# Kernel tuning notes

Measured on AMD Instinct MI355X. Metric: run time of the kernel, lower is better.

## Reference

```python
import jax, jax.numpy as jnp
import numpy as np

L = 4          # num_layers
H = 128        # hidden_channels
F = 128        # num_filters
G = 25         # num_gaussians
N = 10000      # nodes
E = 320000     # radius-graph edges
EH = 40000     # hull edges
NG = 64        # graphs in batch
CUTOFF = 5.0
PI = float(np.pi)
LOG2 = float(np.log(2.0))


def ssp(x):  # ShiftedSoftplus
    return jax.nn.softplus(x) - LOG2


def setup_inputs() -> dict:
    key = jax.random.key(0)
    ks = iter(jax.random.split(key, 64))
    w = lambda shape: jax.random.normal(next(ks), shape, jnp.float32) * 0.05
    inp = {
        'z': jax.random.randint(next(ks), (N,), 0, 100),
        'edge_index': jax.random.randint(next(ks), (2, E), 0, N),
        'edge_index_hull': jax.random.randint(next(ks), (2, EH), 0, N),
        'batch': jnp.sort(jax.random.randint(next(ks), (N,), 0, NG)),
        'dist': jax.random.uniform(next(ks), (E,), jnp.float32) * CUTOFF,
        'fea_hull': jax.random.normal(next(ks), (EH, 7), jnp.float32),
        'emb_table': w((100, H)),
        'lin_w': w((L, F, H)),
        'mlp_w1': w((L, F, G)), 'mlp_b1': jnp.zeros((L, F), jnp.float32),
        'mlp_w2': w((L, F, F)), 'mlp_b2': jnp.zeros((L, F), jnp.float32),
        'linh_w': w((L, F, H)),
        'mlph_w1': w((L, F, 7)), 'mlph_b1': jnp.zeros((L, F), jnp.float32),
        'mlph_w2': w((L, F, F)), 'mlph_b2': jnp.zeros((L, F), jnp.float32),
        'v1_w': w((L, H, F)), 'v1_b': jnp.zeros((L, H), jnp.float32),
        'v2_w': w((L, 64, H)), 'v2_b': jnp.zeros((L, 64), jnp.float32),
        'vh1_w': w((L, H, F)), 'vh1_b': jnp.zeros((L, H), jnp.float32),
        'vh2_w': w((L, 64, H)), 'vh2_b': jnp.zeros((L, 64), jnp.float32),
        'cat_w': w((L, H, 128)), 'cat_b': jnp.zeros((L, H), jnp.float32),
        'u1_w': w((64, H)), 'u1_b': jnp.zeros((64,), jnp.float32),
        'u2_w': w((1, 64)), 'u2_b': jnp.zeros((1,), jnp.float32),
    }
    return inp


def reference(z, edge_index, edge_index_hull, batch, dist, fea_hull, emb_table,
              lin_w, mlp_w1, mlp_b1, mlp_w2, mlp_b2,
              linh_w, mlph_w1, mlph_b1, mlph_w2, mlph_b2,
              v1_w, v1_b, v2_w, v2_b, vh1_w, vh1_b, vh2_w, vh2_b,
              cat_w, cat_b, u1_w, u1_b, u2_w, u2_b):
    n = z.shape[0]
    # Gaussian distance embedding: emb(0, cutoff, G)
    offset = jnp.linspace(0.0, CUTOFF, G)
    coeff = -0.5 / (offset[1] - offset[0]) ** 2
    dist_emb = jnp.exp(coeff * (dist[:, None] - offset[None, :]) ** 2)  # [E,G]
    C = 0.5 * (jnp.cos(dist * PI / CUTOFF) + 1.0)                       # [E]
    j, i = edge_index[0], edge_index[1]
    jh, ih = edge_index_hull[0], edge_index_hull[1]
    v = emb_table[z]                                                    # [N,H]
    for l in range(L):
        # update_e
        W = (ssp(dist_emb @ mlp_w1[l].T + mlp_b1[l]) @ mlp_w2[l].T + mlp_b2[l]) * C[:, None]
        e = (v @ lin_w[l].T)[j] * W                                     # [E,F]
        Wh = ssp(fea_hull @ mlph_w1[l].T + mlph_b1[l]) @ mlph_w2[l].T + mlph_b2[l]
        eh = (v @ linh_w[l].T)[jh] * Wh                                 # [EH,F]
        # update_v
        out = jax.ops.segment_sum(e, i, num_segments=n)
        out = ssp(out @ v1_w[l].T + v1_b[l]) @ v2_w[l].T + v2_b[l]      # [N,64]
        outh = jax.ops.segment_sum(eh, ih, num_segments=n)
        outh = ssp(outh @ vh1_w[l].T + vh1_b[l]) @ vh2_w[l].T + vh2_b[l]
        v = v + ssp(jnp.concatenate([out, outh], axis=1) @ cat_w[l].T + cat_b[l])
    # update_u
    u = ssp(v @ u1_w.T + u1_b) @ u2_w.T + u2_b                          # [N,1]
    return jax.ops.segment_sum(u, batch, num_segments=NG)               # [NG,1]
```

## Files before the change

kernel.cpp:

```cpp
#include <hip/hip_runtime.h>
#include <hip/hip_bf16.h>

typedef __hip_bfloat16 bf16;
typedef unsigned short ushort;
typedef __attribute__((ext_vector_type(8))) short short8;
typedef __attribute__((ext_vector_type(4))) float f32x4;

__device__ __forceinline__ float dssp(float x){
  return fmaxf(x, 0.f) + __logf(1.f + __expf(-fabsf(x))) - 0.693147180559945f;
}
__device__ __forceinline__ int clampi(int x, int lo, int hi){ return x<lo?lo:(x>hi?hi:x); }
__device__ __forceinline__ ushort f2b(float f){
  unsigned x = __float_as_uint(f);
  return (ushort)((x + 0x7fffu + ((x>>16)&1u)) >> 16);
}
__device__ __forceinline__ float b2f16(ushort u){ return __uint_as_float(((unsigned)u)<<16); }

constexpr int TBL_K    = 4096;
constexpr int TBL_ROWS = TBL_K + 1;
constexpr int TBL_TILES = (TBL_ROWS + 31) / 32;

__global__ void detect_mode(const unsigned* __restrict__ raw, int* flag){
  __shared__ int c;
  int t = threadIdx.x;
  if (t==0) c = 0;
  __syncthreads();
  unsigned u  = raw[t];
  unsigned lo = u & 0xFFFFu;
  int e = (int)((lo >> 7) & 0xFF);
  int ok = (lo==0u) || (e >= 0x70 && e <= 0x8F);
  atomicAdd(&c, ok);
  __syncthreads();
  if (t==0) *flag = (c >= 160) ? 1 : 0;
}

struct Seg { const void* src; float* dst; int n; };
struct SegTable { Seg s[27]; int count; long total; };

__global__ void convert_all(SegTable tbl, const int* __restrict__ flag){
  int mode = *flag;
  long tid    = (long)blockIdx.x*blockDim.x + threadIdx.x;
  long stride = (long)gridDim.x*blockDim.x;
  for (long i=tid; i<tbl.total; i+=stride){
    long off = i; int k = 0;
    while (k < tbl.count-1 && off >= tbl.s[k].n){ off -= tbl.s[k].n; k++; }
    float f;
    if (mode) f = __bfloat162float(((const bf16*)tbl.s[k].src)[off]);
    else      f = ((const float*)tbl.s[k].src)[off];
    tbl.s[k].dst[off] = (f==f) ? f : 0.f;
  }
}

struct WSeg { const float* src; ushort* dst; int n; };
struct WTable { WSeg s[9]; int count; int total; };

__global__ void convert_wb(WTable wt){
  int tid = blockIdx.x*blockDim.x + threadIdx.x;
  if (tid >= wt.total) return;
  int off = tid, k = 0;
  while (k < wt.count-1 && off >= wt.s[k].n){ off -= wt.s[k].n; k++; }
  wt.s[k].dst[off] = f2b(wt.s[k].src[off]);
}

__global__ void init_all(int* cnt_r, int* cnt_h, float* uacc,
                         int2* spk_r, int2* spk_h, int N, int E, int EH){
  int t = blockIdx.x*blockDim.x + threadIdx.x;
  if (t < N){ cnt_r[t]=0; cnt_h[t]=0; }
  if (t < 64) uacc[t]=0.f;
  if (t < E)  spk_r[t]=make_int2(0,0);
  if (t < EH) spk_h[t]=make_int2(0,0);
}

__global__ void count_edges(const int* __restrict__ ei, const int* __restrict__ eih,
                            int E, int EH, int N, int* cnt_r, int* cnt_h){
  int t = blockIdx.x*blockDim.x + threadIdx.x;
  if (t < E)  atomicAdd(&cnt_r[clampi(ei[E + t], 0, N-1)], 1);
  if (t < EH) atomicAdd(&cnt_h[clampi(eih[EH + t], 0, N-1)], 1);
}

__global__ __launch_bounds__(256) void scan_pair(const int* cnt_r, int* off_r, int* cur_r,
                                                 const int* cnt_h, int* off_h, int* cur_h, int N){
  __shared__ int s[256];
  int t = threadIdx.x;
  int CH = (N + 255) / 256;
  for (int which=0; which<2; which++){
    const int* cnt = which? cnt_h : cnt_r;
    int* off = which? off_h : off_r;
    int* cur = which? cur_h : cur_r;
    int base = t*CH;
    int sum = 0;
    for (int q=0;q<CH;q++){ int idx=base+q; sum += (idx<N)? cnt[idx] : 0; }
    __syncthreads();
    s[t]=sum; __syncthreads();
    for (int ofs=1; ofs<256; ofs<<=1){
      int v = s[t]; int vp = (t>=ofs)? s[t-ofs] : 0;
      __syncthreads(); s[t]=v+vp; __syncthreads();
    }
    int run = (t>0)? s[t-1] : 0;
    for (int q=0;q<CH;q++){
      int idx=base+q;
      if (idx<N){ off[idx]=run; cur[idx]=run; run += cnt[idx]; }
    }
    if (t==255) off[N] = s[255];
  }
}

__global__ void scatter_edges(const int* __restrict__ ei, const float* __restrict__ distc,
                              const int* __restrict__ eih, int E, int EH, int N,
                              int* cur_r, int* cur_h, int2* spk_r, int2* spk_h){
  int t = blockIdx.x*blockDim.x + threadIdx.x;
  if (t < E){
    int i = clampi(ei[E+t], 0, N-1);
    int p = clampi(atomicAdd(&cur_r[i], 1), 0, E-1);
    float x = fminf(fmaxf(distc[t]*(4096.0f/5.0f), 0.f), 4095.999f);
    int i0 = (int)x; if (i0 > TBL_K-1) i0 = TBL_K-1;
    unsigned fr16 = (unsigned)((x - (float)i0)*65536.0f); if (fr16 > 65535u) fr16 = 65535u;
    spk_r[p] = make_int2(clampi(ei[t],0,N-1), (int)(((unsigned)i0<<16)|fr16));
  }
  if (t < EH){
    int ih = clampi(eih[EH+t], 0, N-1);
    int p = clampi(atomicAdd(&cur_h[ih], 1), 0, EH-1);
    spk_h[p] = make_int2(clampi(eih[t],0,N-1), t);
  }
}

__global__ __launch_bounds__(256) void build_wtab(const float* __restrict__ mlp_w1,
    const float* __restrict__ mlp_b1, const float* __restrict__ mlp_w2,
    const float* __restrict__ mlp_b2, ushort* __restrict__ Wtab){
  int l    = blockIdx.x / TBL_TILES;
  int tile = blockIdx.x % TBL_TILES;
  int row0 = tile * 32;
  const float* w1 = mlp_w1 + l*128*25;
  const float* b1 = mlp_b1 + l*128;
  const float* w2 = mlp_w2 + l*128*128;
  const float* b2 = mlp_b2 + l*128;
  __shared__ float Gs[32][26];
  __shared__ float Ts[32][129];
  __shared__ float Ws[32][129];
  int t = threadIdx.x;
  for (int idx=t; idx<32*25; idx+=256){
    int r = idx/25, k = idx%25;
    float d = (row0+r) * (5.0f/4096.0f);
    float x = d - (float)k*(5.0f/24.0f);
    Gs[r][k] = __expf(-11.52f*x*x);
  }
  __syncthreads();
  int rg = t&7, cg = t>>3;
  #pragma unroll
  for (int ri=0;ri<4;ri++){
    int r = rg*4+ri;
    #pragma unroll
    for (int ci=0;ci<4;ci++){
      int c = cg*4+ci;
      float s = b1[c];
      for (int k=0;k<25;k++) s += Gs[r][k]*w1[c*25+k];
      Ts[r][c] = dssp(s);
    }
  }
  float acc[4][4] = {};
  for (int k0=0;k0<128;k0+=32){
    __syncthreads();
    for (int idx=t; idx<1024; idx+=256){
      int c=idx>>3, kk4=(idx&7)*4;
      float4 f = *(const float4*)(w2+(size_t)c*128+k0+kk4);
      Ws[kk4][c]=f.x; Ws[kk4+1][c]=f.y; Ws[kk4+2][c]=f.z; Ws[kk4+3][c]=f.w;
    }
    __syncthreads();
    for (int kk=0;kk<32;kk++){
      float xv[4];
      #pragma unroll
      for (int ri=0;ri<4;ri++) xv[ri]=Ts[rg*4+ri][k0+kk];
      #pragma unroll
      for (int ci=0;ci<4;ci++){
        float wv = Ws[kk][cg*4+ci];
        #pragma unroll
        for (int ri=0;ri<4;ri++) acc[ri][ci] += xv[ri]*wv;
      }
    }
  }
  #pragma unroll
  for (int ri=0;ri<4;ri++){
    int r = row0 + rg*4 + ri;
    if (r >= TBL_ROWS) continue;
    float d  = r * (5.0f/4096.0f);
    float Cf = 0.5f*(cosf(d*(3.14159265358979f/5.0f))+1.0f);
    #pragma unroll
    for (int ci=0;ci<4;ci++){
      int c = cg*4+ci;
      Wtab[((size_t)l*TBL_ROWS + r)*128 + c] = f2b((acc[ri][ci] + b2[c]) * Cf);
    }
  }
}

__global__ void pack_wtab(const ushort* __restrict__ Wtab, unsigned* __restrict__ Wpk){
  long t = (long)blockIdx.x*blockDim.x + threadIdx.x;
  const long TOT = 4L*TBL_K*128;
  if (t < TOT){
    int l = (int)(t / ((long)TBL_K*128));
    long rem = t % ((long)TBL_K*128);
    int r = (int)(rem >> 7), f = (int)(rem & 127);
    const ushort* base = Wtab + (size_t)l*TBL_ROWS*128;
    Wpk[t] = (((unsigned)base[(size_t)(r+1)*128+f])<<16) | (unsigned)base[(size_t)r*128+f];
  }
}

__device__ __forceinline__ short8 afragb(const ushort (*Xb)[136], int lane, int k0){
  int m=lane&15, q=(lane>>4)&3;
  return *(const short8*)(&Xb[m][k0+q*8]);
}
__device__ __forceinline__ short8 bfrag(const ushort* __restrict__ W, int cbase, int lane, int k0){
  int n=lane&15, q=(lane>>4)&3;
  return *(const short8*)(W + (size_t)(cbase+n)*128 + k0 + q*8);
}
template<int NT>
__device__ __forceinline__ void mgemm(const ushort (*Xb)[136],
    const ushort* __restrict__ W, int t, f32x4 d[NT]){
  int lane=t&63, w=t>>6;
  #pragma unroll
  for (int ct=0;ct<NT;ct++) d[ct]=(f32x4){0.f,0.f,0.f,0.f};
  #pragma unroll
  for (int kc=0;kc<4;kc++){
    short8 a = afragb(Xb, lane, kc*32);
    #pragma unroll
    for (int ct=0;ct<NT;ct++){
      short8 b = bfrag(W, w*(NT*16)+ct*16, lane, kc*32);
      d[ct] = __builtin_amdgcn_mfma_f32_16x16x32_bf16(a, b, d[ct], 0, 0, 0);
    }
  }
}
template<int NT>
__device__ __forceinline__ void d2tile(ushort (*Y)[136], const f32x4 d[NT], int t,
    int colofs, const float* __restrict__ bias, int do_ssp){
  int lane=t&63, w=t>>6, q=(lane>>4)&3, n=lane&15;
  #pragma unroll
  for (int ct=0;ct<NT;ct++){
    int c = w*(NT*16)+ct*16+n;
    float bv = bias? bias[c] : 0.f;
    #pragma unroll
    for (int i=0;i<4;i++){
      float y = d[ct][i] + bv;
      if (do_ssp) y = dssp(y);
      Y[q*4+i][colofs+c] = f2b(y);
    }
  }
}
template<int NT>
__device__ __forceinline__ void d2os(float (*Os)[132], const f32x4 d[NT], int t,
    const float* __restrict__ bias, int do_ssp){
  int lane=t&63, w=t>>6, q=(lane>>4)&3, n=lane&15;
  #pragma unroll
  for (int ct=0;ct<NT;ct++){
    int c = w*(NT*16)+ct*16+n;
    float bv = bias? bias[c] : 0.f;
    #pragma unroll
    for (int i=0;i<4;i++){
      float y = d[ct][i] + bv;
      if (do_ssp) y = dssp(y);
      Os[q*4+i][c] = y;
    }
  }
}
__device__ __forceinline__ void d2glob(ushort* __restrict__ out, const f32x4 d[2],
    int t, int row0, int N){
  int lane=t&63, w=t>>6, q=(lane>>4)&3, n=lane&15;
  #pragma unroll
  for (int ct=0;ct<2;ct++){
    int c = w*32+ct*16+n;
    #pragma unroll
    for (int i=0;i<4;i++){
      int gr = row0 + q*4 + i;
      if (gr<N) out[(size_t)gr*128 + c] = f2b(d[ct][i]);
    }
  }
}

__global__ __launch_bounds__(256) void f_first(const int* __restrict__ z,
    const float* __restrict__ emb, float* __restrict__ v,
    const ushort* __restrict__ linA, const ushort* __restrict__ linB,
    ushort* __restrict__ vlin, ushort* __restrict__ vlinh, int N){
  __shared__ ushort Xb[16][136];
  int t=threadIdx.x; int row0=blockIdx.x*16;
  f32x4 d[2];
  for (int idx=t; idx<512; idx+=256){
    int r=idx>>5, k4=(idx&31)*4; int gr=row0+r;
    int zz=(gr<N)? clampi(z[gr],0,99):0;
    float4 f = *(const float4*)(emb + (size_t)zz*128 + k4);
    unsigned r0 = (unsigned)f2b(f.x) | ((unsigned)f2b(f.y)<<16);
    unsigned r1 = (unsigned)f2b(f.z) | ((unsigned)f2b(f.w)<<16);
    *(uint2*)&Xb[r][k4] = make_uint2(r0,r1);
    if (gr<N) *(float4*)(v + (size_t)gr*128 + k4) = f;
  }
  __syncthreads();
  mgemm<2>(Xb, linA, t, d);
  d2glob(vlin, d, t, row0, N);
  mgemm<2>(Xb, linB, t, d);
  d2glob(vlinh, d, t, row0, N);
}

__global__ __launch_bounds__(256) void f_mid(
    const float* __restrict__ accR, const float* __restrict__ accH,
    float* __restrict__ v,
    const ushort* __restrict__ v1w, const float* __restrict__ v1b,
    const ushort* __restrict__ v2w, const float* __restrict__ v2b,
    const ushort* __restrict__ vh1w, const float* __restrict__ vh1b,
    const ushort* __restrict__ vh2w, const float* __restrict__ vh2b,
    const ushort* __restrict__ cw, const float* __restrict__ cb,
    const ushort* __restrict__ linA, const ushort* __restrict__ linB,
    ushort* __restrict__ vlin, ushort* __restrict__ vlinh, int N){
  __shared__ ushort Xb[16][136];
  __shared__ ushort Xb2[16][136];
  __shared__ ushort Xb3[16][136];
  __shared__ float  Os[16][132];
  int t=threadIdx.x; int row0=blockIdx.x*16;
  f32x4 d[2]; f32x4 d1[1];

  for (int path=0; path<2; path++){
    const float* X = path? accH : accR;
    __syncthreads();
    for (int idx=t; idx<512; idx+=256){
      int r=idx>>5, k4=(idx&31)*4; int gr=row0+r;
      float4 f=(gr<N)? *(const float4*)(X+(size_t)gr*128+k4):make_float4(0,0,0,0);
      unsigned r0 = (unsigned)f2b(f.x) | ((unsigned)f2b(f.y)<<16);
      unsigned r1 = (unsigned)f2b(f.z) | ((unsigned)f2b(f.w)<<16);
      *(uint2*)&Xb[r][k4] = make_uint2(r0,r1);
    }
    __syncthreads();
    mgemm<2>(Xb, path?vh1w:v1w, t, d);
    d2tile<2>(Xb2, d, t, 0, path?vh1b:v1b, 1);
    __syncthreads();
    mgemm<1>(Xb2, path?vh2w:v2w, t, d1);
    d2tile<1>(Xb3, d1, t, path*64, path?vh2b:v2b, 0);
  }
  __syncthreads();
  mgemm<2>(Xb3, cw, t, d);
  d2os<2>(Os, d, t, cb, 1);
  __syncthreads();
  for (int idx=t; idx<512; idx+=256){
    int r=idx>>5, k4=(idx&31)*4; int gr=row0+r;
    float4 f=(gr<N)? *(const float4*)(v+(size_t)gr*128+k4):make_float4(0,0,0,0);
    f.x+=Os[r][k4]; f.y+=Os[r][k4+1]; f.z+=Os[r][k4+2]; f.w+=Os[r][k4+3];
    if (gr<N) *(float4*)(v+(size_t)gr*128+k4)=f;
    unsigned r0 = (unsigned)f2b(f.x) | ((unsigned)f2b(f.y)<<16);
    unsigned r1 = (unsigned)f2b(f.z) | ((unsigned)f2b(f.w)<<16);
    *(uint2*)&Xb[r][k4] = make_uint2(r0,r1);
  }
  __syncthreads();
  mgemm<2>(Xb, linA, t, d);
  d2glob(vlin, d, t, row0, N);
  mgemm<2>(Xb, linB, t, d);
  d2glob(vlinh, d, t, row0, N);
}

__global__ __launch_bounds__(256) void f_last(
    const float* __restrict__ accR, const float* __restrict__ accH,
    const float* __restrict__ v,
    const ushort* __restrict__ v1w, const float* __restrict__ v1b,
    const ushort* __restrict__ v2w, const float* __restrict__ v2b,
    const ushort* __restrict__ vh1w, const float* __restrict__ vh1b,
    const ushort* __restrict__ vh2w, const float* __restrict__ vh2b,
    const ushort* __restrict__ cw, const float* __restrict__ cb,
    const ushort* __restrict__ u1w, const float* __restrict__ u1b,
    const float* __restrict__ u2w, const float* __restrict__ u2b,
    const int* __restrict__ batch, float* __restrict__ uacc, int N){
  __shared__ ushort Xb[16][136];
  __shared__ ushort Xb2[16][136];
  __shared__ ushort Xb3[16][136];
  __shared__ float  Os[16][132];
  __shared__ float ss[16];
  __shared__ int   bb[16];
  int t=threadIdx.x; int row0=blockIdx.x*16;
  f32x4 d[2]; f32x4 d1[1];

  for (int path=0; path<2; path++){
    const float* X = path? accH : accR;
    __syncthreads();
    for (int idx=t; idx<512; idx+=256){
      int r=idx>>5, k4=(idx&31)*4; int gr=row0+r;
      float4 f=(gr<N)? *(const float4*)(X+(size_t)gr*128+k4):make_float4(0,0,0,0);
      unsigned r0 = (unsigned)f2b(f.x) | ((unsigned)f2b(f.y)<<16);
      unsigned r1 = (unsigned)f2b(f.z) | ((unsigned)f2b(f.w)<<16);
      *(uint2*)&Xb[r][k4] = make_uint2(r0,r1);
    }
    __syncthreads();
    mgemm<2>(Xb, path?vh1w:v1w, t, d);
    d2tile<2>(Xb2, d, t, 0, path?vh1b:v1b, 1);
    __syncthreads();
    mgemm<1>(Xb2, path?vh2w:v2w, t, d1);
    d2tile<1>(Xb3, d1, t, path*64, path?vh2b:v2b, 0);
  }
  __syncthreads();
  mgemm<2>(Xb3, cw, t, d);
  d2os<2>(Os, d, t, cb, 1);
  __syncthreads();
  for (int idx=t; idx<512; idx+=256){
    int r=idx>>5, k4=(idx&31)*4; int gr=row0+r;
    float4 f=(gr<N)? *(const float4*)(v+(size_t)gr*128+k4):make_float4(0,0,0,0);
    f.x+=Os[r][k4]; f.y+=Os[r][k4+1]; f.z+=Os[r][k4+2]; f.w+=Os[r][k4+3];
    unsigned r0 = (unsigned)f2b(f.x) | ((unsigned)f2b(f.y)<<16);
    unsigned r1 = (unsigned)f2b(f.z) | ((unsigned)f2b(f.w)<<16);
    *(uint2*)&Xb[r][k4] = make_uint2(r0,r1);
  }
  __syncthreads();
  mgemm<1>(Xb, u1w, t, d1);
  d2os<1>(Os, d1, t, u1b, 1);
  __syncthreads();
  if (t<16){
    int gr=row0+t;
    float s=0.f; int bt=-1;
    if (gr<N){
      s = u2b[0];
      for (int c=0;c<64;c++) s += Os[t][c]*u2w[c];
      bt = clampi(batch[gr],0,63);
    }
    ss[t]=s; bb[t]=bt;
  }
  __syncthreads();
  if (t==0){
    float run=0.f; int cur=-1;
    for (int q=0;q<16;q++){
      int bq=bb[q];
      if (bq<0) continue;
      if (bq!=cur){ if (cur>=0) atomicAdd(&uacc[cur],run); cur=bq; run=0.f; }
      run += ss[q];
    }
    if (cur>=0) atomicAdd(&uacc[cur],run);
  }
}

__global__ __launch_bounds__(256) void hull_all(const int2* __restrict__ spk_h,
    const float* __restrict__ fea,
    const float* __restrict__ mlph_w1, const float* __restrict__ mlph_b1,
    const ushort* __restrict__ mlph_w2b, const float* __restrict__ mlph_b2,
    ushort* __restrict__ WhT_base, size_t lstride, int EHpad,
    int EH, int tilesPerLayer, int l0){
  int l    = l0 + blockIdx.x / tilesPerLayer;
  int tile = blockIdx.x % tilesPerLayer;
  int row0 = tile*64;
  const float* w1 = mlph_w1 + l*128*7;
  const float* b1 = mlph_b1 + l*128;
  const ushort* w2 = mlph_w2b + (size_t)l*16384;
  const float* b2 = mlph_b2 + l*128;
  ushort* WhT = WhT_base + (size_t)(l-l0)*lstride;
  __shared__ float Fs[64][8];
  __shared__ ushort Xb[64][136];
  int t=threadIdx.x;
  for (int idx=t; idx<448; idx+=256){
    int r=idx/7, k=idx%7;
    int p=row0+r;
    int eid=(p<EH)? clampi(spk_h[p].y,0,EH-1):0;
    Fs[r][k]=(p<EH)? fea[(size_t)eid*7+k]:0.f;
  }
  __syncthreads();
  {
    int c0=(t&31)*4, r0=(t>>5)*8;
    float w[4][7]; float bb[4];
    #pragma unroll
    for (int cc=0;cc<4;cc++){
      bb[cc]=b1[c0+cc];
      #pragma unroll
      for (int k=0;k<7;k++) w[cc][k]=w1[(c0+cc)*7+k];
    }
    #pragma unroll
    for (int rr=0;rr<8;rr++){
      int r=r0+rr;
      float fv[7];
      #pragma unroll
      for (int k=0;k<7;k++) fv[k]=Fs[r][k];
      ushort o[4];
      #pragma unroll
      for (int cc=0;cc<4;cc++){
        float s=bb[cc];
        #pragma unroll
        for (int k=0;k<7;k++) s=fmaf(fv[k],w[cc][k],s);
        o[cc]=f2b(dssp(s));
      }
      unsigned lo=(unsigned)o[0]|((unsigned)o[1]<<16);
      unsigned hi=(unsigned)o[2]|((unsigned)o[3]<<16);
      *(uint2*)&Xb[r][c0]=make_uint2(lo,hi);
    }
  }
  __syncthreads();
  int lane=t&63, w=t>>6;
  const ushort (*Xw)[136] = (const ushort (*)[136])&Xb[w*16][0];
  f32x4 d[8];
  #pragma unroll
  for (int ct=0;ct<8;ct++) d[ct]=(f32x4){0.f,0.f,0.f,0.f};
  #pragma unroll
  for (int kc=0;kc<4;kc++){
    short8 a = afragb(Xw, lane, kc*32);
    #pragma unroll
    for (int ct=0;ct<8;ct++){
      short8 b = bfrag(w2, ct*16, lane, kc*32);
      d[ct] = __builtin_amdgcn_mfma_f32_16x16x32_bf16(a, b, d[ct], 0, 0, 0);
    }
  }
  int q=(lane>>4)&3, n=lane&15;
  int p0 = row0 + w*16 + q*4;
  #pragma unroll
  for (int ct=0;ct<8;ct++){
    int c=ct*16+n;
    float bv=b2[c];
    unsigned r0s=(unsigned)f2b(d[ct][0]+bv)|((unsigned)f2b(d[ct][1]+bv)<<16);
    unsigned r1s=(unsigned)f2b(d[ct][2]+bv)|((unsigned)f2b(d[ct][3]+bv)<<16);
    *(uint2*)(WhT + (size_t)c*EHpad + p0) = make_uint2(r0s,r1s);
  }
}

__device__ __forceinline__ float rlerp(unsigned y, const unsigned* __restrict__ Wpk, int f){
  int i0 = (int)(y>>16);
  float fr = (float)(y&0xFFFFu)*(1.f/65536.f);
  unsigned u = Wpk[(size_t)i0*128+f];
  float w0=__uint_as_float(u<<16), w1=__uint_as_float(u&0xFFFF0000u);
  return fmaf(fr, w1-w0, w0);
}

__global__ __launch_bounds__(128) void acc_both(
    const int* __restrict__ off_r, const int2* __restrict__ spk_r,
    const ushort* __restrict__ vlin, const unsigned* __restrict__ Wpk,
    float* __restrict__ accR,
    const int* __restrict__ off_h, const int2* __restrict__ spk_h,
    const ushort* __restrict__ vlinh, const ushort* __restrict__ WhT, int EHpad,
    float* __restrict__ accH,
    int Etot, int EHtot, int N){
  int f = threadIdx.x;
  if ((int)blockIdx.x < N){
    int n = blockIdx.x;
    int b = clampi(off_r[n], 0, Etot);
    int e = clampi(off_r[n+1], b, Etot);
    float a = 0.f;
    int p = b;
    for (; p+4<=e; p+=4){
      int2 k0=spk_r[p], k1=spk_r[p+1], k2=spk_r[p+2], k3=spk_r[p+3];
      float v0 = b2f16(vlin[(size_t)k0.x*128+f]);
      float v1 = b2f16(vlin[(size_t)k1.x*128+f]);
      float v2 = b2f16(vlin[(size_t)k2.x*128+f]);
      float v3 = b2f16(vlin[(size_t)k3.x*128+f]);
      float w0 = rlerp((unsigned)k0.y, Wpk, f);
      float w1 = rlerp((unsigned)k1.y, Wpk, f);
      float w2 = rlerp((unsigned)k2.y, Wpk, f);
      float w3 = rlerp((unsigned)k3.y, Wpk, f);
      a += v0*w0 + v1*w1 + v2*w2 + v3*w3;
    }
    for (; p<e; p++){
      int2 k0=spk_r[p];
      a += b2f16(vlin[(size_t)k0.x*128+f]) * rlerp((unsigned)k0.y, Wpk, f);
    }
    accR[(size_t)n*128+f] = a;
  } else {
    int n = blockIdx.x - N;
    int b = clampi(off_h[n], 0, EHtot);
    int e = clampi(off_h[n+1], b, EHtot);
    const ushort* wrow = WhT + (size_t)f*EHpad;
    float a = 0.f;
    int p = b;
    for (; p+4<=e; p+=4){
      int2 k0=spk_h[p], k1=spk_h[p+1], k2=spk_h[p+2], k3=spk_h[p+3];
      float v0 = b2f16(vlinh[(size_t)k0.x*128+f]);
      float v1 = b2f16(vlinh[(size_t)k1.x*128+f]);
      float v2 = b2f16(vlinh[(size_t)k2.x*128+f]);
      float v3 = b2f16(vlinh[(size_t)k3.x*128+f]);
      a += v0*b2f16(wrow[p]) + v1*b2f16(wrow[p+1]) + v2*b2f16(wrow[p+2]) + v3*b2f16(wrow[p+3]);
    }
    for (; p<e; p++){
      int2 k0=spk_h[p];
      a += b2f16(vlinh[(size_t)k0.x*128+f]) * b2f16(wrow[p]);
    }
    accH[(size_t)n*128+f] = a;
  }
}

__global__ void write_out(const float* __restrict__ uacc, void* out, const int* __restrict__ flag){
  int t = threadIdx.x;
  if (t < 64){
    if (*flag) ((bf16*)out)[t] = __float2bfloat16(uacc[t]);
    else       ((float*)out)[t] = uacc[t];
  }
}

extern "C" void kernel_launch(void* const* d_in, const int* in_sizes, int n_in,
                              void* d_out, int out_size, void* d_ws, size_t ws_size,
                              hipStream_t stream){
  const int* z     = (const int*)d_in[0];
  const int* ei    = (const int*)d_in[1];
  const int* eih   = (const int*)d_in[2];
  const int* batch = (const int*)d_in[3];

  const int N  = in_sizes[0];
  const int E  = in_sizes[1]/2;
  const int EH = in_sizes[2]/2;
  const int EHpad = (EH + 63) & ~63;

  char* wp = (char*)d_ws;
  auto alloc = [&](size_t bytes)->char*{
    char* p = wp; wp += (bytes + 255) & ~(size_t)255; return p;
  };
  int* flag    = (int*)alloc(256);
  int* cnt_r   = (int*)alloc((size_t)N*4);
  int* off_r   = (int*)alloc((size_t)(N+1)*4);
  int* cur_r   = (int*)alloc((size_t)N*4);
  int* cnt_h   = (int*)alloc((size_t)N*4);
  int* off_h   = (int*)alloc((size_t)(N+1)*4);
  int* cur_h   = (int*)alloc((size_t)N*4);
  int2* spk_r  = (int2*)alloc((size_t)E*8);
  int2* spk_h  = (int2*)alloc((size_t)EH*8);
  float* uacc  = (float*)alloc(64*4);

  SegTable tbl; tbl.count = 27; tbl.total = 0;
  float* cvt[27];
  for (int i=0;i<27;i++){
    int n = in_sizes[4+i];
    cvt[i] = (float*)alloc((size_t)n*4);
    tbl.s[i].src = d_in[4+i];
    tbl.s[i].dst = cvt[i];
    tbl.s[i].n   = n;
    tbl.total   += n;
  }
  const float* distc   = cvt[0];
  const float* feac    = cvt[1];
  const float* embc    = cvt[2];
  const float* mlp_w1  = cvt[4];
  const float* mlp_b1  = cvt[5];
  const float* mlp_w2  = cvt[6];
  const float* mlp_b2  = cvt[7];
  const float* mlph_w1 = cvt[9];
  const float* mlph_b1 = cvt[10];
  const float* mlph_b2 = cvt[12];
  const float* v1_b  = cvt[14];
  const float* v2_b  = cvt[16];
  const float* vh1_b = cvt[18];
  const float* vh2_b = cvt[20];
  const float* cat_b = cvt[22];
  const float* u1_b  = cvt[24];
  const float* u2_w  = cvt[25];
  const float* u2_b  = cvt[26];

  ushort* lin_wb   = (ushort*)alloc((size_t)4*16384*2);
  ushort* linh_wb  = (ushort*)alloc((size_t)4*16384*2);
  ushort* v1_wb    = (ushort*)alloc((size_t)4*16384*2);
  ushort* vh1_wb   = (ushort*)alloc((size_t)4*16384*2);
  ushort* cat_wb   = (ushort*)alloc((size_t)4*16384*2);
  ushort* mlph_w2b = (ushort*)alloc((size_t)4*16384*2);
  ushort* v2_wb    = (ushort*)alloc((size_t)4*8192*2);
  ushort* vh2_wb   = (ushort*)alloc((size_t)4*8192*2);
  ushort* u1_wb    = (ushort*)alloc((size_t)8192*2);
  WTable wt; wt.count = 9;
  wt.s[0] = { cvt[3],  lin_wb,   4*16384 };
  wt.s[1] = { cvt[8],  linh_wb,  4*16384 };
  wt.s[2] = { cvt[13], v1_wb,    4*16384 };
  wt.s[3] = { cvt[17], vh1_wb,   4*16384 };
  wt.s[4] = { cvt[21], cat_wb,   4*16384 };
  wt.s[5] = { cvt[11], mlph_w2b, 4*16384 };
  wt.s[6] = { cvt[15], v2_wb,    4*8192  };
  wt.s[7] = { cvt[19], vh2_wb,   4*8192  };
  wt.s[8] = { cvt[23], u1_wb,    8192    };
  wt.total = 6*4*16384 + 2*4*8192 + 8192;

  ushort*   Wtab = (ushort*)alloc((size_t)4*TBL_ROWS*128*2);
  unsigned* Wpk  = (unsigned*)alloc((size_t)4*TBL_K*128*4);
  float* v     = (float*)alloc((size_t)N*128*4);
  ushort* vlin  = (ushort*)alloc((size_t)N*128*2);
  ushort* vlinh = (ushort*)alloc((size_t)N*128*2);
  float* accR  = (float*)alloc((size_t)N*128*4);
  float* accH  = (float*)alloc((size_t)N*128*4);

  size_t used = (size_t)(wp - (char*)d_ws);
  size_t wht1 = (size_t)128*EHpad*2;
  bool pre = (ws_size >= used + 4*wht1 + 256);
  ushort* WhT = (ushort*)alloc(pre ? 4*wht1 : wht1);

  detect_mode<<<1,256,0,stream>>>((const unsigned*)d_in[6], flag);
  {
    int cb = (int)((tbl.total + 255)/256);
    if (cb > 4096) cb = 4096;
    convert_all<<<cb,256,0,stream>>>(tbl, flag);
  }
  convert_wb<<<(wt.total+255)/256,256,0,stream>>>(wt);

  int nb;
  nb = (E+255)/256;     init_all<<<nb,256,0,stream>>>(cnt_r,cnt_h,uacc,spk_r,spk_h,N,E,EH);
  nb = (E+255)/256;     count_edges<<<nb,256,0,stream>>>(ei,eih,E,EH,N,cnt_r,cnt_h);
  scan_pair<<<1,256,0,stream>>>(cnt_r,off_r,cur_r,cnt_h,off_h,cur_h,N);
  nb = (E+255)/256;     scatter_edges<<<nb,256,0,stream>>>(ei,distc,eih,E,EH,N,cur_r,cur_h,spk_r,spk_h);
  build_wtab<<<4*TBL_TILES,256,0,stream>>>(mlp_w1,mlp_b1,mlp_w2,mlp_b2,Wtab);
  pack_wtab<<<(int)((4L*TBL_K*128+255)/256),256,0,stream>>>(Wtab,Wpk);

  const int nt = (N+15)/16;
  const int ht64 = (EH+63)/64;
  if (pre)
    hull_all<<<4*ht64,256,0,stream>>>(spk_h, feac, mlph_w1, mlph_b1, mlph_w2b, mlph_b2,
                                      WhT, (size_t)128*EHpad, EHpad, EH, ht64, 0);

  f_first<<<nt,256,0,stream>>>(z, embc, v, lin_wb, linh_wb, vlin, vlinh, N);
  for (int l=0;l<4;l++){
    if (!pre)
      hull_all<<<ht64,256,0,stream>>>(spk_h, feac, mlph_w1, mlph_b1, mlph_w2b, mlph_b2,
                                      WhT, 0, EHpad, EH, ht64, l);
    const ushort* WhTl = pre ? (WhT + (size_t)l*128*EHpad) : WhT;
    acc_both<<<2*N,128,0,stream>>>(off_r, spk_r, vlin, Wpk + (size_t)l*TBL_K*128, accR,
                                   off_h, spk_h, vlinh, WhTl, EHpad, accH, E, EH, N);
    if (l<3){
      f_mid<<<nt,256,0,stream>>>(accR, accH, v,
          v1_wb + (size_t)l*16384, v1_b + l*128, v2_wb + (size_t)l*8192, v2_b + l*64,
          vh1_wb + (size_t)l*16384, vh1_b + l*128, vh2_wb + (size_t)l*8192, vh2_b + l*64,
          cat_wb + (size_t)l*16384, cat_b + l*128,
          lin_wb + (size_t)(l+1)*16384, linh_wb + (size_t)(l+1)*16384, vlin, vlinh, N);
    } else {
      f_last<<<nt,256,0,stream>>>(accR, accH, v,
          v1_wb + (size_t)l*16384, v1_b + l*128, v2_wb + (size_t)l*8192, v2_b + l*64,
          vh1_wb + (size_t)l*16384, vh1_b + l*128, vh2_wb + (size_t)l*8192, vh2_b + l*64,
          cat_wb + (size_t)l*16384, cat_b + l*128,
          u1_wb, u1_b, u2_w, u2_b, batch, uacc, N);
    }
  }
  write_out<<<1,64,0,stream>>>(uacc, d_out, flag);
}
```

Baseline: 579.5 us.

## Coalesce GEMM output stores via LDS, widen scan, unroll edge gather by eight

```diff
diff --git a/kernel.cpp b/kernel.cpp
--- a/kernel.cpp
+++ b/kernel.cpp
@@ -78,11 +78,11 @@
   if (t < EH) atomicAdd(&cnt_h[clampi(eih[EH + t], 0, N-1)], 1);
 }
 
-__global__ __launch_bounds__(256) void scan_pair(const int* cnt_r, int* off_r, int* cur_r,
-                                                 const int* cnt_h, int* off_h, int* cur_h, int N){
-  __shared__ int s[256];
+__global__ __launch_bounds__(1024) void scan_pair(const int* cnt_r, int* off_r, int* cur_r,
+                                                  const int* cnt_h, int* off_h, int* cur_h, int N){
+  __shared__ int s[1024];
   int t = threadIdx.x;
-  int CH = (N + 255) / 256;
+  int CH = (N + 1023) / 1024;
   for (int which=0; which<2; which++){
     const int* cnt = which? cnt_h : cnt_r;
     int* off = which? off_h : off_r;
@@ -92,7 +92,7 @@
     for (int q=0;q<CH;q++){ int idx=base+q; sum += (idx<N)? cnt[idx] : 0; }
     __syncthreads();
     s[t]=sum; __syncthreads();
-    for (int ofs=1; ofs<256; ofs<<=1){
+    for (int ofs=1; ofs<1024; ofs<<=1){
       int v = s[t]; int vp = (t>=ofs)? s[t-ofs] : 0;
       __syncthreads(); s[t]=v+vp; __syncthreads();
     }
@@ -101,7 +101,7 @@
       int idx=base+q;
       if (idx<N){ off[idx]=run; cur[idx]=run; run += cnt[idx]; }
     }
-    if (t==255) off[N] = s[255];
+    if (t==1023) off[N] = s[1023];
   }
 }
 
@@ -260,18 +260,14 @@
     }
   }
 }
-__device__ __forceinline__ void d2glob(ushort* __restrict__ out, const f32x4 d[2],
-    int t, int row0, int N){
-  int lane=t&63, w=t>>6, q=(lane>>4)&3, n=lane&15;
-  #pragma unroll
-  for (int ct=0;ct<2;ct++){
-    int c = w*32+ct*16+n;
-    #pragma unroll
-    for (int i=0;i<4;i++){
-      int gr = row0 + q*4 + i;
-      if (gr<N) out[(size_t)gr*128 + c] = f2b(d[ct][i]);
-    }
-  }
+__device__ __forceinline__ void d2glob_c(ushort* __restrict__ out, const f32x4 d[2],
+    int t, int row0, int N, ushort (*Tmp)[136]){
+  d2tile<2>(Tmp, d, t, 0, nullptr, 0);
+  __syncthreads();
+  int r=t>>4, o=(t&15)*8;
+  int gr=row0+r;
+  if (gr<N) *(uint4*)(out + (size_t)gr*128 + o) = *(const uint4*)&Tmp[r][o];
+  __syncthreads();
 }
 
 __global__ __launch_bounds__(256) void f_first(const int* __restrict__ z,
@@ -279,6 +275,7 @@
     const ushort* __restrict__ linA, const ushort* __restrict__ linB,
     ushort* __restrict__ vlin, ushort* __restrict__ vlinh, int N){
   __shared__ ushort Xb[16][136];
+  __shared__ ushort Tb[16][136];
   int t=threadIdx.x; int row0=blockIdx.x*16;
   f32x4 d[2];
   for (int idx=t; idx<512; idx+=256){
@@ -292,9 +289,9 @@
   }
   __syncthreads();
   mgemm<2>(Xb, linA, t, d);
-  d2glob(vlin, d, t, row0, N);
+  d2glob_c(vlin, d, t, row0, N, Tb);
   mgemm<2>(Xb, linB, t, d);
-  d2glob(vlinh, d, t, row0, N);
+  d2glob_c(vlinh, d, t, row0, N, Tb);
 }
 
 __global__ __launch_bounds__(256) void f_mid(
@@ -346,9 +343,9 @@
   }
   __syncthreads();
   mgemm<2>(Xb, linA, t, d);
-  d2glob(vlin, d, t, row0, N);
+  d2glob_c(vlin, d, t, row0, N, Xb2);
   mgemm<2>(Xb, linB, t, d);
-  d2glob(vlinh, d, t, row0, N);
+  d2glob_c(vlinh, d, t, row0, N, Xb2);
 }
 
 __global__ __launch_bounds__(256) void f_last(
@@ -441,14 +438,20 @@
   const ushort* w2 = mlph_w2b + (size_t)l*16384;
   const float* b2 = mlph_b2 + l*128;
   ushort* WhT = WhT_base + (size_t)(l-l0)*lstride;
+  __shared__ int   Eid[64];
   __shared__ float Fs[64][8];
   __shared__ ushort Xb[64][136];
+  __shared__ ushort Ys[128][70];
   int t=threadIdx.x;
+  if (t < 64){
+    int p=row0+t;
+    Eid[t]=(p<EH)? clampi(spk_h[p].y,0,EH-1):0;
+  }
+  __syncthreads();
   for (int idx=t; idx<448; idx+=256){
     int r=idx/7, k=idx%7;
     int p=row0+r;
-    int eid=(p<EH)? clampi(spk_h[p].y,0,EH-1):0;
-    Fs[r][k]=(p<EH)? fea[(size_t)eid*7+k]:0.f;
+    Fs[r][k]=(p<EH)? fea[(size_t)Eid[r]*7+k]:0.f;
   }
   __syncthreads();
   {
@@ -495,14 +498,20 @@
     }
   }
   int q=(lane>>4)&3, n=lane&15;
-  int p0 = row0 + w*16 + q*4;
   #pragma unroll
   for (int ct=0;ct<8;ct++){
     int c=ct*16+n;
     float bv=b2[c];
     unsigned r0s=(unsigned)f2b(d[ct][0]+bv)|((unsigned)f2b(d[ct][1]+bv)<<16);
     unsigned r1s=(unsigned)f2b(d[ct][2]+bv)|((unsigned)f2b(d[ct][3]+bv)<<16);
-    *(uint2*)(WhT + (size_t)c*EHpad + p0) = make_uint2(r0s,r1s);
+    *(uint2*)&Ys[c][w*16+q*4] = make_uint2(r0s,r1s);
+  }
+  __syncthreads();
+  #pragma unroll
+  for (int j=0;j<4;j++){
+    int col = j*32 + (t>>3);
+    int r0  = (t&7)*8;
+    *(uint4*)(WhT + (size_t)col*EHpad + row0 + r0) = *(const uint4*)&Ys[col][r0];
   }
 }
 
@@ -529,6 +538,18 @@
     int e = clampi(off_r[n+1], b, Etot);
     float a = 0.f;
     int p = b;
+    for (; p+8<=e; p+=8){
+      int2 k[8];
+      #pragma unroll
+      for (int j=0;j<8;j++) k[j]=spk_r[p+j];
+      float vv[8], ww[8];
+      #pragma unroll
+      for (int j=0;j<8;j++) vv[j]=b2f16(vlin[(size_t)k[j].x*128+f]);
+      #pragma unroll
+      for (int j=0;j<8;j++) ww[j]=rlerp((unsigned)k[j].y, Wpk, f);
+      #pragma unroll
+      for (int j=0;j<8;j++) a=fmaf(vv[j],ww[j],a);
+    }
     for (; p+4<=e; p+=4){
       int2 k0=spk_r[p], k1=spk_r[p+1], k2=spk_r[p+2], k3=spk_r[p+3];
       float v0 = b2f16(vlin[(size_t)k0.x*128+f]);
@@ -679,7 +700,7 @@
   int nb;
   nb = (E+255)/256;     init_all<<<nb,256,0,stream>>>(cnt_r,cnt_h,uacc,spk_r,spk_h,N,E,EH);
   nb = (E+255)/256;     count_edges<<<nb,256,0,stream>>>(ei,eih,E,EH,N,cnt_r,cnt_h);
-  scan_pair<<<1,256,0,stream>>>(cnt_r,off_r,cur_r,cnt_h,off_h,cur_h,N);
+  scan_pair<<<1,1024,0,stream>>>(cnt_r,off_r,cur_r,cnt_h,off_h,cur_h,N);
   nb = (E+255)/256;     scatter_edges<<<nb,256,0,stream>>>(ei,distc,eih,E,EH,N,cur_r,cur_h,spk_r,spk_h);
   build_wtab<<<4*TBL_TILES,256,0,stream>>>(mlp_w1,mlp_b1,mlp_w2,mlp_b2,Wtab);
   pack_wtab<<<(int)((4L*TBL_K*128+255)/256),256,0,stream>>>(Wtab,Wpk);
```

Measured after the change: 532.3 us. 8.2% less time.
